# Optimization experiments

Hardware: AMD Instinct MI355X
Metric: run time of the kernel (lower is better)

Reference implementation:

```python
import jax, jax.numpy as jnp
import numpy as np

B, L, D, H = 2, 128, 256, 256
BASE_LR = 0.01
LR_SHIFT = float(np.log(np.expm1(BASE_LR)))  # log(expm1(base_lr))


def silu_backward(x):
    s = jax.nn.silu(x)
    return s + jax.nn.sigmoid(x) * (1.0 - s)


def decay_matrix(log_g):
    # log_g: [B,L] -> M[b,l,m] = exp(sum_{i=m+1..l} log_g[b,i]) for m<=l, else 0
    n = log_g.shape[1]
    strict = jnp.tril(jnp.ones((n, n), log_g.dtype), -1)
    cum = jnp.cumsum(log_g[:, :, None] * strict, axis=1)
    return jnp.exp(cum) * jnp.tril(jnp.ones((n, n), log_g.dtype))


def setup_inputs():
    key = jax.random.key(0)
    ks = jax.random.split(key, 22)
    p = lambda k, shape: jax.random.normal(k, shape, jnp.float32) * 0.02
    inp = {
        'x': jax.random.normal(ks[0], (B, L, D), jnp.float32),
        'Wq': p(ks[1], (D, D)), 'bq': p(ks[2], (D,)),
        'Wk': p(ks[3], (D, D)), 'bk': p(ks[4], (D,)),
        'Wv': p(ks[5], (D, D)), 'bv': p(ks[6], (D,)),
        'Wlr': p(ks[7], (D, 1)), 'blr': p(ks[8], (1,)),
        'Wm': p(ks[9], (D, 1)), 'bm': p(ks[10], (1,)),
        'Wd': p(ks[11], (D, 1)), 'bd': p(ks[12], (1,)),
        'W1': p(ks[13], (B, H, D)), 'b1': p(ks[14], (B, H)),
        'W2': p(ks[15], (B, D, H)), 'b2': p(ks[16], (B, D)),
        'mW1': p(ks[17], (B, H, D)), 'mb1': p(ks[18], (B, H)),
        'mW2': p(ks[19], (B, D, H)), 'mb2': p(ks[20], (B, D)),
    }
    return inp


def reference(x, Wq, bq, Wk, bk, Wv, bv, Wlr, blr, Wm, bm, Wd, bd,
              W1, b1, W2, b2, mW1, mb1, mW2, mb2):
    query = x @ Wq + bq
    key_ = x @ Wk + bk
    value = x @ Wv + bv

    # forward through fast-weight MLP at current (chunk-start) weights
    Z1 = jnp.einsum('bhd,bld->blh', W1, key_) + b1[:, None, :]
    X2 = jax.nn.silu(Z1)
    Z2 = jnp.einsum('bdh,blh->bld', W2, X2) + b2[:, None, :]

    # per-token gradients of 0.5*||Z2 - value||^2
    grad_Z2 = Z2 - value
    grad_b2 = grad_Z2
    grad_W2 = jnp.einsum('bld,blh->bldh', grad_Z2, X2)
    grad_X2 = jnp.einsum('bld,bdh->blh', grad_Z2, W2)
    grad_Z1 = grad_X2 * silu_backward(Z1)
    grad_b1 = grad_Z1
    grad_W1 = jnp.einsum('blh,bld->blhd', grad_Z1, key_)

    lr = jax.nn.softplus((x @ Wlr).squeeze(-1) + blr + LR_SHIFT)  # [B,L]
    gW1 = grad_W1 * lr[:, :, None, None]
    gb1 = grad_b1 * lr[:, :, None]
    gW2 = grad_W2 * lr[:, :, None, None]
    gb2 = grad_b2 * lr[:, :, None]

    # momentum recurrence (decay-gated linear scan, materialized as LxL matrix)
    fc_mom = (x @ Wm).squeeze(-1) + bm  # [B,L]
    log_mom = -jax.nn.softplus(-fc_mom)
    M = decay_matrix(log_mom)  # [B,L,L]
    mom_cum = jnp.exp(jnp.cumsum(log_mom, axis=1))  # [B,L]

    mgW1 = jnp.einsum('blm,bmhd->blhd', M, gW1) - jnp.einsum('bl,bhd->blhd', mom_cum, mW1)
    mgb1 = jnp.einsum('blm,bmh->blh', M, gb1) - jnp.einsum('bl,bh->blh', mom_cum, mb1)
    mgW2 = jnp.einsum('blm,bmdh->bldh', M, gW2) - jnp.einsum('bl,bdh->bldh', mom_cum, mW2)
    mgb2 = jnp.einsum('blm,bmd->bld', M, gb2) - jnp.einsum('bl,bd->bld', mom_cum, mb2)

    # weight-decay recurrence
    log_wd = -jax.nn.softplus((x @ Wd).squeeze(-1) + bd)  # [B,L]
    Dm = decay_matrix(log_wd)
    wd_cum = jnp.exp(jnp.cumsum(log_wd, axis=1))

    W1p = jnp.einsum('blm,bmhd->blhd', Dm, mgW1) + jnp.einsum('bl,bhd->blhd', wd_cum, W1)
    b1p = jnp.einsum('blm,bmh->blh', Dm, mgb1) + jnp.einsum('bl,bh->blh', wd_cum, b1)
    W2p = jnp.einsum('blm,bmdh->bldh', Dm, mgW2) + jnp.einsum('bl,bdh->bldh', wd_cum, W2)
    b2p = jnp.einsum('blm,bmd->bld', Dm, mgb2) + jnp.einsum('bl,bd->bld', wd_cum, b2)

    # query pass through per-token updated weights
    Zq1 = jnp.einsum('blhd,bld->blh', W1p, query) + b1p
    Zq2 = jnp.einsum('bldh,blh->bld', W2p, jax.nn.silu(Zq1)) + b2p

    return (Zq2,
            W1p[:, -1], b1p[:, -1], W2p[:, -1], b2p[:, -1],
            mgW1[:, -1], mgb1[:, -1], mgW2[:, -1], mgb2[:, -1])
```

## Files before the change

### kernel.cpp

```cpp
#include <hip/hip_runtime.h>
#include <hip/hip_bf16.h>
#include <math.h>

constexpr int Bn = 2, Ln = 128, Dn = 256, Hn = 256;

#define LR_SHIFT (-4.6001660040607144f)

constexpr int OFF_Q      = 0;
constexpr int OFF_K      = 65536;
constexpr int OFF_V      = 131072;
constexpr int OFF_X2     = 196608;
constexpr int OFF_GZ1    = 262144;
constexpr int OFF_GZ2    = 327680;
constexpr int OFF_XQ     = 393216;
constexpr int OFF_KT     = 458752;
constexpr int OFF_A      = 524288;
constexpr int OFF_W1T    = 557056;
constexpr int OFF_W2T    = 688128;
constexpr int OFF_MW1T   = 819200;
constexpr int OFF_MW2T   = 950272;
constexpr int OFF_LR     = 1081344;
constexpr int OFF_PM     = 1081600;
constexpr int OFF_PD     = 1081856;
constexpr int OFF_MOMCUM = 1082112;
constexpr int OFF_WDCUM  = 1082368;
constexpr int OFF_C      = 1082624;
constexpr int OFF_LOGM   = 1082880;
constexpr int OFF_LOGWD  = 1083136;
constexpr int OFF_X2T    = 1083392;

constexpr int OUT_ZQ2  = 0;
constexpr int OUT_W1P  = 65536;
constexpr int OUT_B1P  = 196608;
constexpr int OUT_W2P  = 197120;
constexpr int OUT_B2P  = 328192;
constexpr int OUT_MGW1 = 328704;
constexpr int OUT_MGB1 = 459776;
constexpr int OUT_MGW2 = 460288;
constexpr int OUT_MGB2 = 591360;

__device__ __forceinline__ float softplus_f(float z) {
    return fmaxf(z, 0.0f) + log1pf(expf(-fabsf(z)));
}

__device__ __forceinline__ float4 fma4(float s, const float4 w, float4 a) {
    a.x += s * w.x; a.y += s * w.y; a.z += s * w.z; a.w += s * w.w; return a;
}

__global__ __launch_bounds__(256) void transpose_kernel(
    const float* __restrict__ W1, const float* __restrict__ W2,
    const float* __restrict__ mW1, const float* __restrict__ mW2,
    float* __restrict__ ws) {
    int z = blockIdx.z; int mat = z >> 1; int b = z & 1;
    const float* src; float* dst;
    if (mat == 0)      { src = W1  + b * 65536; dst = ws + OFF_W1T  + b * 65536; }
    else if (mat == 1) { src = W2  + b * 65536; dst = ws + OFF_W2T  + b * 65536; }
    else if (mat == 2) { src = mW1 + b * 65536; dst = ws + OFF_MW1T + b * 65536; }
    else               { src = mW2 + b * 65536; dst = ws + OFF_MW2T + b * 65536; }
    __shared__ float tile[32][33];
    int tx = threadIdx.x & 31, ty = threadIdx.x >> 5;
    int r0 = blockIdx.y * 32, c0 = blockIdx.x * 32;
    for (int i = 0; i < 32; i += 8)
        tile[ty + i][tx] = src[(r0 + ty + i) * 256 + (c0 + tx)];
    __syncthreads();
    for (int i = 0; i < 32; i += 8)
        dst[(c0 + ty + i) * 256 + (r0 + tx)] = tile[tx][ty + i];
}

__global__ __launch_bounds__(256) void proj_kernel(
    const float* __restrict__ x,
    const float* __restrict__ Wq, const float* __restrict__ bq,
    const float* __restrict__ Wk, const float* __restrict__ bk,
    const float* __restrict__ Wv, const float* __restrict__ bv,
    const float* __restrict__ Wlr, const float* __restrict__ blr,
    const float* __restrict__ Wm, const float* __restrict__ bm,
    const float* __restrict__ Wd, const float* __restrict__ bd,
    float* __restrict__ ws) {
    int bl = blockIdx.x;
    int t = threadIdx.x;
    int o = t & 63, dl = t >> 6;
    __shared__ float xs[256];
    __shared__ float rq[1024], rk[1024], rv[1024];
    xs[t] = x[bl * 256 + t];
    __syncthreads();

    float4 aq = {0, 0, 0, 0}, ak = {0, 0, 0, 0}, av = {0, 0, 0, 0};
#pragma unroll 4
    for (int i = 0; i < 64; ++i) {
        int d = dl + 4 * i;
        float xv = xs[d];
        aq = fma4(xv, *(const float4*)(Wq + d * 256 + 4 * o), aq);
        ak = fma4(xv, *(const float4*)(Wk + d * 256 + 4 * o), ak);
        av = fma4(xv, *(const float4*)(Wv + d * 256 + 4 * o), av);
    }
    *(float4*)(rq + dl * 256 + 4 * o) = aq;
    *(float4*)(rk + dl * 256 + 4 * o) = ak;
    *(float4*)(rv + dl * 256 + 4 * o) = av;
    __syncthreads();
    float q = rq[t] + rq[256 + t] + rq[512 + t] + rq[768 + t] + bq[t];
    float k = rk[t] + rk[256 + t] + rk[512 + t] + rk[768 + t] + bk[t];
    float v = rv[t] + rv[256 + t] + rv[512 + t] + rv[768 + t] + bv[t];
    ws[OFF_Q + bl * 256 + t] = q;
    ws[OFF_K + bl * 256 + t] = k;
    ws[OFF_V + bl * 256 + t] = v;
    __syncthreads();

    rq[t] = xs[t] * Wlr[t];
    rk[t] = xs[t] * Wm[t];
    rv[t] = xs[t] * Wd[t];
    __syncthreads();
    for (int s = 128; s > 0; s >>= 1) {
        if (t < s) { rq[t] += rq[t + s]; rk[t] += rk[t + s]; rv[t] += rv[t + s]; }
        __syncthreads();
    }
    if (t == 0) {
        ws[OFF_LR + bl]    = softplus_f(rq[0] + blr[0] + LR_SHIFT);
        ws[OFF_LOGM + bl]  = -softplus_f(-(rk[0] + bm[0]));
        ws[OFF_LOGWD + bl] = -softplus_f(rv[0] + bd[0]);
    }
}

__global__ __launch_bounds__(128) void scan_kernel(float* __restrict__ ws) {
    int b = blockIdx.x; int t = threadIdx.x;
    __shared__ float sm[128], sd[128], se[128];
    sm[t] = ws[OFF_LOGM + b * Ln + t];
    sd[t] = ws[OFF_LOGWD + b * Ln + t];
    __syncthreads();
    for (int off = 1; off < 128; off <<= 1) {
        float am = (t >= off) ? sm[t - off] : 0.0f;
        float ad = (t >= off) ? sd[t - off] : 0.0f;
        __syncthreads();
        sm[t] += am; sd[t] += ad;
        __syncthreads();
    }
    float pm = sm[t], pd = sd[t];
    ws[OFF_PM + b * Ln + t] = pm;
    ws[OFF_PD + b * Ln + t] = pd;
    ws[OFF_MOMCUM + b * Ln + t] = expf(pm);
    ws[OFF_WDCUM + b * Ln + t]  = expf(pd);
    se[t] = expf(pm - pd);
    __syncthreads();
    for (int off = 1; off < 128; off <<= 1) {
        float a = (t >= off) ? se[t - off] : 0.0f;
        __syncthreads();
        se[t] += a;
        __syncthreads();
    }
    ws[OFF_C + b * Ln + t] = expf(pd) * se[t];
}

__global__ __launch_bounds__(128) void a_kernel(float* __restrict__ ws) {
    int bl = blockIdx.x; int b = bl >> 7; int l = bl & 127;
    int m1 = threadIdx.x;
    const float* Pm = ws + OFF_PM + b * Ln;
    const float* Pd = ws + OFF_PD + b * Ln;
    float a = 0.0f;
    if (m1 <= l) {
        float pdl = Pd[l], pmm1 = Pm[m1];
        float s = 0.0f;
        for (int m = m1; m <= l; ++m)
            s += expf((pdl - Pd[m]) + (Pm[m] - pmm1));
        a = s;
    }
    ws[OFF_A + bl * Ln + m1] = a;
}

__global__ __launch_bounds__(256) void fwd_kernel(
    const float* __restrict__ W2g, const float* __restrict__ b1,
    const float* __restrict__ b2, float* __restrict__ ws) {
    int bl = blockIdx.x, b = bl >> 7, t = threadIdx.x;
    int o = t & 63, dl = t >> 6;
    __shared__ float ks[256], x2s[256], gz2s[256], red[1024];
    const float* W1t = ws + OFF_W1T + b * 65536;
    const float* W2t = ws + OFF_W2T + b * 65536;
    const float* W2n = W2g + b * 65536;
    ks[t] = ws[OFF_K + bl * 256 + t];
    __syncthreads();

    float4 a1 = {0, 0, 0, 0};
#pragma unroll 8
    for (int i = 0; i < 64; ++i) {
        int d = dl + 4 * i;
        a1 = fma4(ks[d], *(const float4*)(W1t + d * 256 + 4 * o), a1);
    }
    *(float4*)(red + dl * 256 + 4 * o) = a1;
    __syncthreads();
    float z1 = red[t] + red[256 + t] + red[512 + t] + red[768 + t] + b1[b * 256 + t];
    float sg = 1.0f / (1.0f + expf(-z1));
    float x2 = z1 * sg;
    ws[OFF_X2 + bl * 256 + t] = x2;
    x2s[t] = x2;
    __syncthreads();

    float4 a2 = {0, 0, 0, 0};
#pragma unroll 8
    for (int i = 0; i < 64; ++i) {
        int h = dl + 4 * i;
        a2 = fma4(x2s[h], *(const float4*)(W2t + h * 256 + 4 * o), a2);
    }
    *(float4*)(red + dl * 256 + 4 * o) = a2;
    __syncthreads();
    float z2 = red[t] + red[256 + t] + red[512 + t] + red[768 + t] + b2[b * 256 + t];
    float gz2 = z2 - ws[OFF_V + bl * 256 + t];
    ws[OFF_GZ2 + bl * 256 + t] = gz2;
    gz2s[t] = gz2;
    __syncthreads();

    float4 a3 = {0, 0, 0, 0};
#pragma unroll 8
    for (int i = 0; i < 64; ++i) {
        int d = dl + 4 * i;
        a3 = fma4(gz2s[d], *(const float4*)(W2n + d * 256 + 4 * o), a3);
    }
    *(float4*)(red + dl * 256 + 4 * o) = a3;
    __syncthreads();
    float gx2 = red[t] + red[256 + t] + red[512 + t] + red[768 + t];
    float gz1 = gx2 * (x2 + sg * (1.0f - x2));
    ws[OFF_GZ1 + bl * 256 + t] = gz1;
}

__global__ __launch_bounds__(256) void transpkx_kernel(float* __restrict__ ws) {
    int z = blockIdx.z; int b = z & 1; int mat = z >> 1;
    const float* src = ws + (mat ? OFF_X2 : OFF_K) + b * 32768;
    float* dst = ws + (mat ? OFF_X2T : OFF_KT) + b * 32768;
    __shared__ float tile[32][33];
    int tx = threadIdx.x & 31, ty = threadIdx.x >> 5;
    int l0 = blockIdx.y * 32, n0 = blockIdx.x * 32;
    for (int i = 0; i < 32; i += 8)
        tile[ty + i][tx] = src[(l0 + ty + i) * 256 + (n0 + tx)];
    __syncthreads();
    for (int i = 0; i < 32; i += 8)
        dst[(n0 + ty + i) * 128 + (l0 + tx)] = tile[tx][ty + i];
}

__global__ __launch_bounds__(256) void zq1_kernel(
    const float* __restrict__ b1, const float* __restrict__ mb1,
    float* __restrict__ ws) {
    int bl = blockIdx.x, b = bl >> 7, l = bl & 127, t = threadIdx.x;
    int o = t & 63, dl = t >> 6, m4 = t & 31, sl = t >> 5;
    __shared__ float qs[256], ps[128], red[1024], ru[1024], rv[1024];
    qs[t] = ws[OFF_Q + bl * 256 + t];
    __syncthreads();

    const float* Kt = ws + OFF_KT + b * 32768;
    float4 as = {0, 0, 0, 0};
#pragma unroll 8
    for (int i = 0; i < 32; ++i) {
        int d = sl + 8 * i;
        as = fma4(qs[d], *(const float4*)(Kt + d * 128 + 4 * m4), as);
    }
    *(float4*)(red + sl * 128 + 4 * m4) = as;
    __syncthreads();
    if (t < 128) {
        float s = 0.0f;
#pragma unroll
        for (int j = 0; j < 8; ++j) s += red[j * 128 + t];
        float p = 0.0f;
        if (t <= l)
            p = ws[OFF_A + bl * Ln + t] * ws[OFF_LR + b * Ln + t] * (1.0f + s);
        ps[t] = p;
    }
    __syncthreads();

    const float* W1t  = ws + OFF_W1T  + b * 65536;
    const float* mW1t = ws + OFF_MW1T + b * 65536;
    float4 au = {0, 0, 0, 0}, av = {0, 0, 0, 0};
#pragma unroll 4
    for (int i = 0; i < 64; ++i) {
        int d = dl + 4 * i;
        float qd = qs[d];
        au = fma4(qd, *(const float4*)(W1t  + d * 256 + 4 * o), au);
        av = fma4(qd, *(const float4*)(mW1t + d * 256 + 4 * o), av);
    }
    *(float4*)(ru + dl * 256 + 4 * o) = au;
    *(float4*)(rv + dl * 256 + 4 * o) = av;

    const float* gz1p = ws + OFF_GZ1 + b * 32768;
    float accp = 0.0f;
#pragma unroll 4
    for (int m = 0; m <= l; ++m) accp += ps[m] * gz1p[m * 256 + t];
    __syncthreads();
    float u = ru[t] + ru[256 + t] + ru[512 + t] + ru[768 + t];
    float v = rv[t] + rv[256 + t] + rv[512 + t] + rv[768 + t];
    float cl = ws[OFF_C + b * Ln + l];
    float wd = ws[OFF_WDCUM + b * Ln + l];
    float z = accp - cl * (v + mb1[b * 256 + t]) + wd * (u + b1[b * 256 + t]);
    float sg = 1.0f / (1.0f + expf(-z));
    ws[OFF_XQ + bl * 256 + t] = z * sg;
}

__global__ __launch_bounds__(256) void zq2_kernel(
    const float* __restrict__ b2, const float* __restrict__ mb2,
    float* __restrict__ out, float* __restrict__ ws) {
    int bl = blockIdx.x, b = bl >> 7, l = bl & 127, t = threadIdx.x;
    int o = t & 63, dl = t >> 6, m4 = t & 31, sl = t >> 5;
    __shared__ float xqs[256], ps[128], red[1024], ru[1024], rv[1024];
    xqs[t] = ws[OFF_XQ + bl * 256 + t];
    __syncthreads();

    const float* X2t = ws + OFF_X2T + b * 32768;
    float4 as = {0, 0, 0, 0};
#pragma unroll 8
    for (int i = 0; i < 32; ++i) {
        int h = sl + 8 * i;
        as = fma4(xqs[h], *(const float4*)(X2t + h * 128 + 4 * m4), as);
    }
    *(float4*)(red + sl * 128 + 4 * m4) = as;
    __syncthreads();
    if (t < 128) {
        float s = 0.0f;
#pragma unroll
        for (int j = 0; j < 8; ++j) s += red[j * 128 + t];
        float p = 0.0f;
        if (t <= l)
            p = ws[OFF_A + bl * Ln + t] * ws[OFF_LR + b * Ln + t] * (1.0f + s);
        ps[t] = p;
    }
    __syncthreads();

    const float* W2t  = ws + OFF_W2T  + b * 65536;
    const float* mW2t = ws + OFF_MW2T + b * 65536;
    float4 au = {0, 0, 0, 0}, av = {0, 0, 0, 0};
#pragma unroll 4
    for (int i = 0; i < 64; ++i) {
        int h = dl + 4 * i;
        float xh = xqs[h];
        au = fma4(xh, *(const float4*)(W2t  + h * 256 + 4 * o), au);
        av = fma4(xh, *(const float4*)(mW2t + h * 256 + 4 * o), av);
    }
    *(float4*)(ru + dl * 256 + 4 * o) = au;
    *(float4*)(rv + dl * 256 + 4 * o) = av;

    const float* gz2p = ws + OFF_GZ2 + b * 32768;
    float accp = 0.0f;
#pragma unroll 4
    for (int m = 0; m <= l; ++m) accp += ps[m] * gz2p[m * 256 + t];
    __syncthreads();
    float u = ru[t] + ru[256 + t] + ru[512 + t] + ru[768 + t];
    float v = rv[t] + rv[256 + t] + rv[512 + t] + rv[768 + t];
    float cl = ws[OFF_C + b * Ln + l];
    float wd = ws[OFF_WDCUM + b * Ln + l];
    out[OUT_ZQ2 + bl * 256 + t] =
        accp - cl * (v + mb2[b * 256 + t]) + wd * (u + b2[b * 256 + t]);
}

__global__ __launch_bounds__(256) void lastw_kernel(
    const float* __restrict__ W1, const float* __restrict__ mW1,
    const float* __restrict__ W2, const float* __restrict__ mW2,
    const float* __restrict__ ws, float* __restrict__ out) {
    int z = blockIdx.z; int b = z >> 1; int fam = z & 1;
    int t = threadIdx.x;
    __shared__ float wa[128], wm[128];
    __shared__ float LA[128][16], LM[128][16], R[128][16];
    const float* lr = ws + OFF_LR + b * Ln;
    const float* Pm = ws + OFF_PM + b * Ln;
    const float* Arow = ws + OFF_A + (b * Ln + Ln - 1) * Ln;
    if (t < 128) {
        wa[t] = Arow[t] * lr[t];
        wm[t] = expf(Pm[Ln - 1] - Pm[t]) * lr[t];
    }
    const float* left  = ws + (fam == 0 ? OFF_GZ1 : OFF_GZ2) + b * Ln * 256;
    const float* right = ws + (fam == 0 ? OFF_K   : OFF_X2 ) + b * Ln * 256;
    int i0 = blockIdx.y * 16, j0 = blockIdx.x * 16;
    __syncthreads();
    for (int e = t; e < 2048; e += 256) {
        int m = e >> 4, i = e & 15;
        float lv = left[m * 256 + i0 + i];
        LA[m][i] = wa[m] * lv;
        LM[m][i] = wm[m] * lv;
        R[m][i]  = right[m * 256 + j0 + i];
    }
    __syncthreads();
    int tx = t & 15, ty = t >> 4;
    float accA = 0.0f, accM = 0.0f;
#pragma unroll 4
    for (int m = 0; m < 128; ++m) {
        accA += LA[m][ty] * R[m][tx];
        accM += LM[m][ty] * R[m][tx];
    }
    float c_last  = ws[OFF_C + b * Ln + Ln - 1];
    float wd_last = ws[OFF_WDCUM + b * Ln + Ln - 1];
    float mc_last = ws[OFF_MOMCUM + b * Ln + Ln - 1];
    int i = i0 + ty, j = j0 + tx;
    const float* base1 = (fam == 0 ? W1 : W2) + b * 65536;
    const float* basem = (fam == 0 ? mW1 : mW2) + b * 65536;
    float b1v = base1[i * 256 + j], bmv = basem[i * 256 + j];
    int op = (fam == 0 ? OUT_W1P : OUT_W2P) + (b * 256 + i) * 256 + j;
    int om = (fam == 0 ? OUT_MGW1 : OUT_MGW2) + (b * 256 + i) * 256 + j;
    out[op] = accA - c_last * bmv + wd_last * b1v;
    out[om] = accM - mc_last * bmv;
}

__global__ __launch_bounds__(256) void lastb_kernel(
    const float* __restrict__ b1, const float* __restrict__ mb1,
    const float* __restrict__ b2, const float* __restrict__ mb2,
    const float* __restrict__ ws, float* __restrict__ out) {
    int b = blockIdx.x; int t = threadIdx.x;
    __shared__ float wa[128], wm[128];
    if (t < 128) {
        wa[t] = ws[OFF_A + (b * Ln + Ln - 1) * Ln + t] * ws[OFF_LR + b * Ln + t];
        wm[t] = expf(ws[OFF_PM + b * Ln + Ln - 1] - ws[OFF_PM + b * Ln + t]) *
                ws[OFF_LR + b * Ln + t];
    }
    __syncthreads();
    const float* gz1 = ws + OFF_GZ1 + b * Ln * 256;
    const float* gz2 = ws + OFF_GZ2 + b * Ln * 256;
    float sA1 = 0, sM1 = 0, sA2 = 0, sM2 = 0;
#pragma unroll 4
    for (int m = 0; m < 128; ++m) {
        float g1 = gz1[m * 256 + t], g2 = gz2[m * 256 + t];
        sA1 += wa[m] * g1; sM1 += wm[m] * g1;
        sA2 += wa[m] * g2; sM2 += wm[m] * g2;
    }
    float c_last  = ws[OFF_C + b * Ln + Ln - 1];
    float wd_last = ws[OFF_WDCUM + b * Ln + Ln - 1];
    float mc_last = ws[OFF_MOMCUM + b * Ln + Ln - 1];
    out[OUT_B1P + b * 256 + t]  = sA1 - c_last * mb1[b * 256 + t] + wd_last * b1[b * 256 + t];
    out[OUT_MGB1 + b * 256 + t] = sM1 - mc_last * mb1[b * 256 + t];
    out[OUT_B2P + b * 256 + t]  = sA2 - c_last * mb2[b * 256 + t] + wd_last * b2[b * 256 + t];
    out[OUT_MGB2 + b * 256 + t] = sM2 - mc_last * mb2[b * 256 + t];
}

extern "C" void kernel_launch(void* const* d_in, const int* in_sizes, int n_in,
                              void* d_out, int out_size, void* d_ws, size_t ws_size,
                              hipStream_t stream) {
    const float* x   = (const float*)d_in[0];
    const float* Wq  = (const float*)d_in[1];
    const float* bq  = (const float*)d_in[2];
    const float* Wk  = (const float*)d_in[3];
    const float* bk  = (const float*)d_in[4];
    const float* Wv  = (const float*)d_in[5];
    const float* bv  = (const float*)d_in[6];
    const float* Wlr = (const float*)d_in[7];
    const float* blr = (const float*)d_in[8];
    const float* Wm  = (const float*)d_in[9];
    const float* bm  = (const float*)d_in[10];
    const float* Wd  = (const float*)d_in[11];
    const float* bd  = (const float*)d_in[12];
    const float* W1  = (const float*)d_in[13];
    const float* b1  = (const float*)d_in[14];
    const float* W2  = (const float*)d_in[15];
    const float* b2  = (const float*)d_in[16];
    const float* mW1 = (const float*)d_in[17];
    const float* mb1 = (const float*)d_in[18];
    const float* mW2 = (const float*)d_in[19];
    const float* mb2 = (const float*)d_in[20];
    float* ws  = (float*)d_ws;
    float* out = (float*)d_out;

    transpose_kernel<<<dim3(8, 8, 8), 256, 0, stream>>>(W1, W2, mW1, mW2, ws);
    proj_kernel<<<Bn * Ln, 256, 0, stream>>>(x, Wq, bq, Wk, bk, Wv, bv,
                                             Wlr, blr, Wm, bm, Wd, bd, ws);
    scan_kernel<<<Bn, 128, 0, stream>>>(ws);
    a_kernel<<<Bn * Ln, 128, 0, stream>>>(ws);
    fwd_kernel<<<Bn * Ln, 256, 0, stream>>>(W2, b1, b2, ws);
    transpkx_kernel<<<dim3(8, 4, 4), 256, 0, stream>>>(ws);
    zq1_kernel<<<Bn * Ln, 256, 0, stream>>>(b1, mb1, ws);
    zq2_kernel<<<Bn * Ln, 256, 0, stream>>>(b2, mb2, out, ws);
    lastw_kernel<<<dim3(16, 16, Bn * 2), 256, 0, stream>>>(W1, mW1, W2, mW2, ws, out);
    lastb_kernel<<<Bn, 256, 0, stream>>>(b1, mb1, b2, mb2, ws, out);
}
```

Baseline: 237.5 us.

## Tile projection and query-pass GEMMs over 8-token blocks to reuse weight loads

```diff
diff --git a/kernel.cpp b/kernel.cpp
--- a/kernel.cpp
+++ b/kernel.cpp
@@ -1,5 +1,4 @@
 #include <hip/hip_runtime.h>
-#include <hip/hip_bf16.h>
 #include <math.h>
 
 constexpr int Bn = 2, Ln = 128, Dn = 256, Hn = 256;
@@ -47,6 +46,10 @@
     a.x += s * w.x; a.y += s * w.y; a.z += s * w.z; a.w += s * w.w; return a;
 }
 
+__device__ __forceinline__ float silu_f(float z) {
+    return z / (1.0f + expf(-z));
+}
+
 __global__ __launch_bounds__(256) void transpose_kernel(
     const float* __restrict__ W1, const float* __restrict__ W2,
     const float* __restrict__ mW1, const float* __restrict__ mW2,
@@ -67,56 +70,63 @@
         dst[(c0 + ty + i) * 256 + (r0 + tx)] = tile[tx][ty + i];
 }
 
-__global__ __launch_bounds__(256) void proj_kernel(
+__global__ __launch_bounds__(128) void qkv_kernel(
     const float* __restrict__ x,
     const float* __restrict__ Wq, const float* __restrict__ bq,
     const float* __restrict__ Wk, const float* __restrict__ bk,
     const float* __restrict__ Wv, const float* __restrict__ bv,
+    float* __restrict__ ws) {
+    int mat = blockIdx.z;
+    const float* W    = (mat == 0) ? Wq : (mat == 1) ? Wk : Wv;
+    const float* bias = (mat == 0) ? bq : (mat == 1) ? bk : bv;
+    int outoff = (mat == 0) ? OFF_Q : (mat == 1) ? OFF_K : OFF_V;
+    int bl0 = blockIdx.y * 8;
+    int c0  = blockIdx.x * 64;
+    int t = threadIdx.x;
+    __shared__ float xs[8][260];
+    for (int i = t; i < 512; i += 128) {
+        int tok = i >> 6, kq = i & 63;
+        *(float4*)&xs[tok][kq * 4] = *(const float4*)(x + (bl0 + tok) * 256 + kq * 4);
+    }
+    __syncthreads();
+    int tok = t >> 4, cq = t & 15;
+    int c = c0 + 4 * cq;
+    const float* Wp = W + c;
+    float4 acc = {0, 0, 0, 0};
+#pragma unroll 8
+    for (int k = 0; k < 256; ++k)
+        acc = fma4(xs[tok][k], *(const float4*)(Wp + k * 256), acc);
+    float4 bb = *(const float4*)(bias + c);
+    acc.x += bb.x; acc.y += bb.y; acc.z += bb.z; acc.w += bb.w;
+    *(float4*)(ws + outoff + (bl0 + tok) * 256 + c) = acc;
+}
+
+__global__ __launch_bounds__(256) void scalproj_kernel(
+    const float* __restrict__ x,
     const float* __restrict__ Wlr, const float* __restrict__ blr,
     const float* __restrict__ Wm, const float* __restrict__ bm,
     const float* __restrict__ Wd, const float* __restrict__ bd,
     float* __restrict__ ws) {
-    int bl = blockIdx.x;
-    int t = threadIdx.x;
-    int o = t & 63, dl = t >> 6;
-    __shared__ float xs[256];
-    __shared__ float rq[1024], rk[1024], rv[1024];
-    xs[t] = x[bl * 256 + t];
-    __syncthreads();
-
-    float4 aq = {0, 0, 0, 0}, ak = {0, 0, 0, 0}, av = {0, 0, 0, 0};
-#pragma unroll 4
-    for (int i = 0; i < 64; ++i) {
-        int d = dl + 4 * i;
-        float xv = xs[d];
-        aq = fma4(xv, *(const float4*)(Wq + d * 256 + 4 * o), aq);
-        ak = fma4(xv, *(const float4*)(Wk + d * 256 + 4 * o), ak);
-        av = fma4(xv, *(const float4*)(Wv + d * 256 + 4 * o), av);
-    }
-    *(float4*)(rq + dl * 256 + 4 * o) = aq;
-    *(float4*)(rk + dl * 256 + 4 * o) = ak;
-    *(float4*)(rv + dl * 256 + 4 * o) = av;
-    __syncthreads();
-    float q = rq[t] + rq[256 + t] + rq[512 + t] + rq[768 + t] + bq[t];
-    float k = rk[t] + rk[256 + t] + rk[512 + t] + rk[768 + t] + bk[t];
-    float v = rv[t] + rv[256 + t] + rv[512 + t] + rv[768 + t] + bv[t];
-    ws[OFF_Q + bl * 256 + t] = q;
-    ws[OFF_K + bl * 256 + t] = k;
-    ws[OFF_V + bl * 256 + t] = v;
-    __syncthreads();
-
-    rq[t] = xs[t] * Wlr[t];
-    rk[t] = xs[t] * Wm[t];
-    rv[t] = xs[t] * Wd[t];
-    __syncthreads();
-    for (int s = 128; s > 0; s >>= 1) {
-        if (t < s) { rq[t] += rq[t + s]; rk[t] += rk[t + s]; rv[t] += rv[t + s]; }
-        __syncthreads();
-    }
-    if (t == 0) {
-        ws[OFF_LR + bl]    = softplus_f(rq[0] + blr[0] + LR_SHIFT);
-        ws[OFF_LOGM + bl]  = -softplus_f(-(rk[0] + bm[0]));
-        ws[OFF_LOGWD + bl] = -softplus_f(rv[0] + bd[0]);
+    int t = threadIdx.x;
+    int ln = t & 63, wv = t >> 6;
+    int bl = blockIdx.x * 4 + wv;
+    float4 xv = *(const float4*)(x + bl * 256 + ln * 4);
+    float4 wl = *(const float4*)(Wlr + ln * 4);
+    float4 wm = *(const float4*)(Wm + ln * 4);
+    float4 wd = *(const float4*)(Wd + ln * 4);
+    float s1 = xv.x * wl.x + xv.y * wl.y + xv.z * wl.z + xv.w * wl.w;
+    float s2 = xv.x * wm.x + xv.y * wm.y + xv.z * wm.z + xv.w * wm.w;
+    float s3 = xv.x * wd.x + xv.y * wd.y + xv.z * wd.z + xv.w * wd.w;
+#pragma unroll
+    for (int off = 32; off > 0; off >>= 1) {
+        s1 += __shfl_xor(s1, off);
+        s2 += __shfl_xor(s2, off);
+        s3 += __shfl_xor(s3, off);
+    }
+    if (ln == 0) {
+        ws[OFF_LR + bl]    = softplus_f(s1 + blr[0] + LR_SHIFT);
+        ws[OFF_LOGM + bl]  = -softplus_f(-(s2 + bm[0]));
+        ws[OFF_LOGWD + bl] = -softplus_f(s3 + bd[0]);
     }
 }
 
@@ -165,58 +175,59 @@
     ws[OFF_A + bl * Ln + m1] = a;
 }
 
-__global__ __launch_bounds__(256) void fwd_kernel(
-    const float* __restrict__ W2g, const float* __restrict__ b1,
+template <int MODE>
+__global__ __launch_bounds__(128) void fstage_kernel(
+    const float* __restrict__ W2nat, const float* __restrict__ b1,
     const float* __restrict__ b2, float* __restrict__ ws) {
-    int bl = blockIdx.x, b = bl >> 7, t = threadIdx.x;
-    int o = t & 63, dl = t >> 6;
-    __shared__ float ks[256], x2s[256], gz2s[256], red[1024];
-    const float* W1t = ws + OFF_W1T + b * 65536;
-    const float* W2t = ws + OFF_W2T + b * 65536;
-    const float* W2n = W2g + b * 65536;
-    ks[t] = ws[OFF_K + bl * 256 + t];
-    __syncthreads();
-
-    float4 a1 = {0, 0, 0, 0};
+    int bl0 = blockIdx.y * 8;
+    int b = bl0 >> 7;
+    int c0 = blockIdx.x * 64;
+    const float* in; const float* W;
+    if (MODE == 0)      { in = ws + OFF_K;   W = ws + OFF_W1T + b * 65536; }
+    else if (MODE == 1) { in = ws + OFF_X2;  W = ws + OFF_W2T + b * 65536; }
+    else                { in = ws + OFF_GZ2; W = W2nat + b * 65536; }
+    int t = threadIdx.x;
+    __shared__ float xs[8][260];
+    for (int i = t; i < 512; i += 128) {
+        int tok = i >> 6, kq = i & 63;
+        *(float4*)&xs[tok][kq * 4] = *(const float4*)(in + (bl0 + tok) * 256 + kq * 4);
+    }
+    __syncthreads();
+    int tok = t >> 4, cq = t & 15;
+    int c = c0 + 4 * cq;
+    const float* Wp = W + c;
+    float4 acc = {0, 0, 0, 0};
 #pragma unroll 8
-    for (int i = 0; i < 64; ++i) {
-        int d = dl + 4 * i;
-        a1 = fma4(ks[d], *(const float4*)(W1t + d * 256 + 4 * o), a1);
-    }
-    *(float4*)(red + dl * 256 + 4 * o) = a1;
-    __syncthreads();
-    float z1 = red[t] + red[256 + t] + red[512 + t] + red[768 + t] + b1[b * 256 + t];
-    float sg = 1.0f / (1.0f + expf(-z1));
-    float x2 = z1 * sg;
-    ws[OFF_X2 + bl * 256 + t] = x2;
-    x2s[t] = x2;
-    __syncthreads();
-
-    float4 a2 = {0, 0, 0, 0};
-#pragma unroll 8
-    for (int i = 0; i < 64; ++i) {
-        int h = dl + 4 * i;
-        a2 = fma4(x2s[h], *(const float4*)(W2t + h * 256 + 4 * o), a2);
-    }
-    *(float4*)(red + dl * 256 + 4 * o) = a2;
-    __syncthreads();
-    float z2 = red[t] + red[256 + t] + red[512 + t] + red[768 + t] + b2[b * 256 + t];
-    float gz2 = z2 - ws[OFF_V + bl * 256 + t];
-    ws[OFF_GZ2 + bl * 256 + t] = gz2;
-    gz2s[t] = gz2;
-    __syncthreads();
-
-    float4 a3 = {0, 0, 0, 0};
-#pragma unroll 8
-    for (int i = 0; i < 64; ++i) {
-        int d = dl + 4 * i;
-        a3 = fma4(gz2s[d], *(const float4*)(W2n + d * 256 + 4 * o), a3);
-    }
-    *(float4*)(red + dl * 256 + 4 * o) = a3;
-    __syncthreads();
-    float gx2 = red[t] + red[256 + t] + red[512 + t] + red[768 + t];
-    float gz1 = gx2 * (x2 + sg * (1.0f - x2));
-    ws[OFF_GZ1 + bl * 256 + t] = gz1;
+    for (int k = 0; k < 256; ++k)
+        acc = fma4(xs[tok][k], *(const float4*)(Wp + k * 256), acc);
+    int row = (bl0 + tok) * 256 + c;
+    if (MODE == 0) {
+        float4 bb = *(const float4*)(b1 + b * 256 + c);
+        float4 z = {acc.x + bb.x, acc.y + bb.y, acc.z + bb.z, acc.w + bb.w};
+        *(float4*)(ws + OFF_GZ1 + row) = z;
+        float4 s = {silu_f(z.x), silu_f(z.y), silu_f(z.z), silu_f(z.w)};
+        *(float4*)(ws + OFF_X2 + row) = s;
+    } else if (MODE == 1) {
+        float4 bb = *(const float4*)(b2 + b * 256 + c);
+        float4 v = *(const float4*)(ws + OFF_V + row);
+        float4 g = {acc.x + bb.x - v.x, acc.y + bb.y - v.y,
+                    acc.z + bb.z - v.z, acc.w + bb.w - v.w};
+        *(float4*)(ws + OFF_GZ2 + row) = g;
+    } else {
+        float4 z = *(const float4*)(ws + OFF_GZ1 + row);
+        float4 g;
+        {
+            float sg = 1.0f / (1.0f + expf(-z.x));
+            g.x = acc.x * (sg * (1.0f + z.x * (1.0f - sg)));
+            sg = 1.0f / (1.0f + expf(-z.y));
+            g.y = acc.y * (sg * (1.0f + z.y * (1.0f - sg)));
+            sg = 1.0f / (1.0f + expf(-z.z));
+            g.z = acc.z * (sg * (1.0f + z.z * (1.0f - sg)));
+            sg = 1.0f / (1.0f + expf(-z.w));
+            g.w = acc.w * (sg * (1.0f + z.w * (1.0f - sg)));
+        }
+        *(float4*)(ws + OFF_GZ1 + row) = g;
+    }
 }
 
 __global__ __launch_bounds__(256) void transpkx_kernel(float* __restrict__ ws) {
@@ -233,115 +244,136 @@
         dst[(n0 + ty + i) * 128 + (l0 + tx)] = tile[tx][ty + i];
 }
 
-__global__ __launch_bounds__(256) void zq1_kernel(
+__global__ __launch_bounds__(128) void zq1_kernel(
     const float* __restrict__ b1, const float* __restrict__ mb1,
     float* __restrict__ ws) {
-    int bl = blockIdx.x, b = bl >> 7, l = bl & 127, t = threadIdx.x;
-    int o = t & 63, dl = t >> 6, m4 = t & 31, sl = t >> 5;
-    __shared__ float qs[256], ps[128], red[1024], ru[1024], rv[1024];
-    qs[t] = ws[OFF_Q + bl * 256 + t];
-    __syncthreads();
-
-    const float* Kt = ws + OFF_KT + b * 32768;
-    float4 as = {0, 0, 0, 0};
-#pragma unroll 8
-    for (int i = 0; i < 32; ++i) {
-        int d = sl + 8 * i;
-        as = fma4(qs[d], *(const float4*)(Kt + d * 128 + 4 * m4), as);
-    }
-    *(float4*)(red + sl * 128 + 4 * m4) = as;
-    __syncthreads();
-    if (t < 128) {
-        float s = 0.0f;
+    int b = blockIdx.z;
+    int l0 = blockIdx.y * 8;
+    int c0 = blockIdx.x * 64;
+    int t = threadIdx.x;
+    __shared__ float qs[8][260];
+    __shared__ float ps[8][132];
+    for (int i = t; i < 512; i += 128) {
+        int tok = i >> 6, kq = i & 63;
+        *(float4*)&qs[tok][kq * 4] =
+            *(const float4*)(ws + OFF_Q + (b * 128 + l0 + tok) * 256 + kq * 4);
+    }
+    __syncthreads();
+    {
+        int m = t;
+        float sv[8] = {0, 0, 0, 0, 0, 0, 0, 0};
+        const float* KT = ws + OFF_KT + b * 32768;
+#pragma unroll 4
+        for (int d = 0; d < 256; ++d) {
+            float kv = KT[d * 128 + m];
 #pragma unroll
-        for (int j = 0; j < 8; ++j) s += red[j * 128 + t];
-        float p = 0.0f;
-        if (t <= l)
-            p = ws[OFF_A + bl * Ln + t] * ws[OFF_LR + b * Ln + t] * (1.0f + s);
-        ps[t] = p;
-    }
-    __syncthreads();
-
-    const float* W1t  = ws + OFF_W1T  + b * 65536;
-    const float* mW1t = ws + OFF_MW1T + b * 65536;
+            for (int j = 0; j < 8; ++j) sv[j] += qs[j][d] * kv;
+        }
+        float lrm = ws[OFF_LR + b * 128 + m];
+#pragma unroll
+        for (int j = 0; j < 8; ++j) {
+            int l = l0 + j;
+            float p = 0.0f;
+            if (m <= l)
+                p = ws[OFF_A + (b * 128 + l) * 128 + m] * lrm * (1.0f + sv[j]);
+            ps[j][m] = p;
+        }
+    }
+    __syncthreads();
+    int tok = t >> 4, cq = t & 15;
+    int c = c0 + 4 * cq;
+    const float* W1t  = ws + OFF_W1T  + b * 65536 + c;
+    const float* mW1t = ws + OFF_MW1T + b * 65536 + c;
     float4 au = {0, 0, 0, 0}, av = {0, 0, 0, 0};
 #pragma unroll 4
-    for (int i = 0; i < 64; ++i) {
-        int d = dl + 4 * i;
-        float qd = qs[d];
-        au = fma4(qd, *(const float4*)(W1t  + d * 256 + 4 * o), au);
-        av = fma4(qd, *(const float4*)(mW1t + d * 256 + 4 * o), av);
-    }
-    *(float4*)(ru + dl * 256 + 4 * o) = au;
-    *(float4*)(rv + dl * 256 + 4 * o) = av;
-
-    const float* gz1p = ws + OFF_GZ1 + b * 32768;
-    float accp = 0.0f;
-#pragma unroll 4
-    for (int m = 0; m <= l; ++m) accp += ps[m] * gz1p[m * 256 + t];
-    __syncthreads();
-    float u = ru[t] + ru[256 + t] + ru[512 + t] + ru[768 + t];
-    float v = rv[t] + rv[256 + t] + rv[512 + t] + rv[768 + t];
-    float cl = ws[OFF_C + b * Ln + l];
-    float wd = ws[OFF_WDCUM + b * Ln + l];
-    float z = accp - cl * (v + mb1[b * 256 + t]) + wd * (u + b1[b * 256 + t]);
-    float sg = 1.0f / (1.0f + expf(-z));
-    ws[OFF_XQ + bl * 256 + t] = z * sg;
-}
-
-__global__ __launch_bounds__(256) void zq2_kernel(
+    for (int d = 0; d < 256; ++d) {
+        float qd = qs[tok][d];
+        au = fma4(qd, *(const float4*)(W1t + d * 256), au);
+        av = fma4(qd, *(const float4*)(mW1t + d * 256), av);
+    }
+    float4 ap = {0, 0, 0, 0};
+    const float* gz1p = ws + OFF_GZ1 + b * 32768 + c;
+    int mmax = l0 + 8;
+#pragma unroll 4
+    for (int m = 0; m < mmax; ++m)
+        ap = fma4(ps[tok][m], *(const float4*)(gz1p + m * 256), ap);
+    int l = l0 + tok;
+    float cl = ws[OFF_C + b * 128 + l];
+    float wd = ws[OFF_WDCUM + b * 128 + l];
+    float4 mb = *(const float4*)(mb1 + b * 256 + c);
+    float4 bb = *(const float4*)(b1 + b * 256 + c);
+    float4 o;
+    o.x = silu_f(ap.x - cl * (av.x + mb.x) + wd * (au.x + bb.x));
+    o.y = silu_f(ap.y - cl * (av.y + mb.y) + wd * (au.y + bb.y));
+    o.z = silu_f(ap.z - cl * (av.z + mb.z) + wd * (au.z + bb.z));
+    o.w = silu_f(ap.w - cl * (av.w + mb.w) + wd * (au.w + bb.w));
+    *(float4*)(ws + OFF_XQ + (b * 128 + l) * 256 + c) = o;
+}
+
+__global__ __launch_bounds__(128) void zq2_kernel(
     const float* __restrict__ b2, const float* __restrict__ mb2,
     float* __restrict__ out, float* __restrict__ ws) {
-    int bl = blockIdx.x, b = bl >> 7, l = bl & 127, t = threadIdx.x;
-    int o = t & 63, dl = t >> 6, m4 = t & 31, sl = t >> 5;
-    __shared__ float xqs[256], ps[128], red[1024], ru[1024], rv[1024];
-    xqs[t] = ws[OFF_XQ + bl * 256 + t];
-    __syncthreads();
-
-    const float* X2t = ws + OFF_X2T + b * 32768;
-    float4 as = {0, 0, 0, 0};
-#pragma unroll 8
-    for (int i = 0; i < 32; ++i) {
-        int h = sl + 8 * i;
-        as = fma4(xqs[h], *(const float4*)(X2t + h * 128 + 4 * m4), as);
-    }
-    *(float4*)(red + sl * 128 + 4 * m4) = as;
-    __syncthreads();
-    if (t < 128) {
-        float s = 0.0f;
+    int b = blockIdx.z;
+    int l0 = blockIdx.y * 8;
+    int c0 = blockIdx.x * 64;
+    int t = threadIdx.x;
+    __shared__ float xqs[8][260];
+    __shared__ float ps[8][132];
+    for (int i = t; i < 512; i += 128) {
+        int tok = i >> 6, kq = i & 63;
+        *(float4*)&xqs[tok][kq * 4] =
+            *(const float4*)(ws + OFF_XQ + (b * 128 + l0 + tok) * 256 + kq * 4);
+    }
+    __syncthreads();
+    {
+        int m = t;
+        float sv[8] = {0, 0, 0, 0, 0, 0, 0, 0};
+        const float* X2t = ws + OFF_X2T + b * 32768;
+#pragma unroll 4
+        for (int h = 0; h < 256; ++h) {
+            float xv = X2t[h * 128 + m];
 #pragma unroll
-        for (int j = 0; j < 8; ++j) s += red[j * 128 + t];
-        float p = 0.0f;
-        if (t <= l)
-            p = ws[OFF_A + bl * Ln + t] * ws[OFF_LR + b * Ln + t] * (1.0f + s);
-        ps[t] = p;
-    }
-    __syncthreads();
-
-    const float* W2t  = ws + OFF_W2T  + b * 65536;
-    const float* mW2t = ws + OFF_MW2T + b * 65536;
+            for (int j = 0; j < 8; ++j) sv[j] += xqs[j][h] * xv;
+        }
+        float lrm = ws[OFF_LR + b * 128 + m];
+#pragma unroll
+        for (int j = 0; j < 8; ++j) {
+            int l = l0 + j;
+            float p = 0.0f;
+            if (m <= l)
+                p = ws[OFF_A + (b * 128 + l) * 128 + m] * lrm * (1.0f + sv[j]);
+            ps[j][m] = p;
+        }
+    }
+    __syncthreads();
+    int tok = t >> 4, cq = t & 15;
+    int c = c0 + 4 * cq;
+    const float* W2t  = ws + OFF_W2T  + b * 65536 + c;
+    const float* mW2t = ws + OFF_MW2T + b * 65536 + c;
     float4 au = {0, 0, 0, 0}, av = {0, 0, 0, 0};
 #pragma unroll 4
-    for (int i = 0; i < 64; ++i) {
-        int h = dl + 4 * i;
-        float xh = xqs[h];
-        au = fma4(xh, *(const float4*)(W2t  + h * 256 + 4 * o), au);
-        av = fma4(xh, *(const float4*)(mW2t + h * 256 + 4 * o), av);
-    }
-    *(float4*)(ru + dl * 256 + 4 * o) = au;
-    *(float4*)(rv + dl * 256 + 4 * o) = av;
-
-    const float* gz2p = ws + OFF_GZ2 + b * 32768;
-    float accp = 0.0f;
-#pragma unroll 4
-    for (int m = 0; m <= l; ++m) accp += ps[m] * gz2p[m * 256 + t];
-    __syncthreads();
-    float u = ru[t] + ru[256 + t] + ru[512 + t] + ru[768 + t];
-    float v = rv[t] + rv[256 + t] + rv[512 + t] + rv[768 + t];
-    float cl = ws[OFF_C + b * Ln + l];
-    float wd = ws[OFF_WDCUM + b * Ln + l];
-    out[OUT_ZQ2 + bl * 256 + t] =
-        accp - cl * (v + mb2[b * 256 + t]) + wd * (u + b2[b * 256 + t]);
+    for (int h = 0; h < 256; ++h) {
+        float xh = xqs[tok][h];
+        au = fma4(xh, *(const float4*)(W2t + h * 256), au);
+        av = fma4(xh, *(const float4*)(mW2t + h * 256), av);
+    }
+    float4 ap = {0, 0, 0, 0};
+    const float* gz2p = ws + OFF_GZ2 + b * 32768 + c;
+    int mmax = l0 + 8;
+#pragma unroll 4
+    for (int m = 0; m < mmax; ++m)
+        ap = fma4(ps[tok][m], *(const float4*)(gz2p + m * 256), ap);
+    int l = l0 + tok;
+    float cl = ws[OFF_C + b * 128 + l];
+    float wd = ws[OFF_WDCUM + b * 128 + l];
+    float4 mb = *(const float4*)(mb2 + b * 256 + c);
+    float4 bb = *(const float4*)(b2 + b * 256 + c);
+    float4 o;
+    o.x = ap.x - cl * (av.x + mb.x) + wd * (au.x + bb.x);
+    o.y = ap.y - cl * (av.y + mb.y) + wd * (au.y + bb.y);
+    o.z = ap.z - cl * (av.z + mb.z) + wd * (au.z + bb.z);
+    o.w = ap.w - cl * (av.w + mb.w) + wd * (au.w + bb.w);
+    *(float4*)(out + OUT_ZQ2 + (b * 128 + l) * 256 + c) = o;
 }
 
 __global__ __launch_bounds__(256) void lastw_kernel(
@@ -449,14 +481,16 @@
     float* out = (float*)d_out;
 
     transpose_kernel<<<dim3(8, 8, 8), 256, 0, stream>>>(W1, W2, mW1, mW2, ws);
-    proj_kernel<<<Bn * Ln, 256, 0, stream>>>(x, Wq, bq, Wk, bk, Wv, bv,
-                                             Wlr, blr, Wm, bm, Wd, bd, ws);
+    qkv_kernel<<<dim3(4, 32, 3), 128, 0, stream>>>(x, Wq, bq, Wk, bk, Wv, bv, ws);
+    scalproj_kernel<<<64, 256, 0, stream>>>(x, Wlr, blr, Wm, bm, Wd, bd, ws);
     scan_kernel<<<Bn, 128, 0, stream>>>(ws);
     a_kernel<<<Bn * Ln, 128, 0, stream>>>(ws);
-    fwd_kernel<<<Bn * Ln, 256, 0, stream>>>(W2, b1, b2, ws);
+    fstage_kernel<0><<<dim3(4, 32), 128, 0, stream>>>(W2, b1, b2, ws);
+    fstage_kernel<1><<<dim3(4, 32), 128, 0, stream>>>(W2, b1, b2, ws);
+    fstage_kernel<2><<<dim3(4, 32), 128, 0, stream>>>(W2, b1, b2, ws);
     transpkx_kernel<<<dim3(8, 4, 4), 256, 0, stream>>>(ws);
-    zq1_kernel<<<Bn * Ln, 256, 0, stream>>>(b1, mb1, ws);
-    zq2_kernel<<<Bn * Ln, 256, 0, stream>>>(b2, mb2, out, ws);
+    zq1_kernel<<<dim3(4, 16, 2), 128, 0, stream>>>(b1, mb1, ws);
+    zq2_kernel<<<dim3(4, 16, 2), 128, 0, stream>>>(b2, mb2, out, ws);
     lastw_kernel<<<dim3(16, 16, Bn * 2), 256, 0, stream>>>(W1, mW1, W2, mW2, ws, out);
     lastb_kernel<<<Bn, 256, 0, stream>>>(b1, mb1, b2, mb2, ws, out);
 }
```

Result: slower. 295.8 us (+24.6%).
